# Kernel tuning notes

Measured on AMD Instinct MI355X. Metric: run time of the kernel, lower is better.

## Reference

```python
import jax, jax.numpy as jnp
import numpy as np

B, N, D, H, L = 16, 1024, 256, 128, 2  # batch, nodes, feat dim, gcn_hidden, n_layers (D == 2*H)


def setup_inputs() -> dict:
    key = jax.random.key(0)
    ks = jax.random.split(key, 16)
    inp = {
        "gcn_input": jax.random.normal(ks[0], (B, N, D), jnp.float32),
        # scale adjacencies by 1/N so aggregated features stay O(1)
        "latent_adj": jax.random.uniform(ks[1], (B, N, N), jnp.float32) / N,
        "dep_adj": jax.random.uniform(ks[2], (B, N, N), jnp.float32) / N,
        # stacked per-layer parameters (leading dim L); layers share shapes since D == 2*H
        "refine_gate": jax.random.normal(ks[3], (L, D, 1), jnp.float32) * 0.02,
        "gate_W_in": jax.random.normal(ks[4], (L, D, 1), jnp.float32) * 0.02,
        "gate_b_in": jnp.zeros((L, 1), jnp.float32),
        "gate_W_out": jax.random.normal(ks[5], (L, D, 1), jnp.float32) * 0.02,
        "gate_b_out": jnp.zeros((L, 1), jnp.float32),
        "fc_in_W": jax.random.normal(ks[6], (L, H, D), jnp.float32) * 0.02,
        "fc_in_b": jnp.zeros((L, H), jnp.float32),
        "fc_out_W": jax.random.normal(ks[7], (L, H, D), jnp.float32) * 0.02,
        "fc_out_b": jnp.zeros((L, H), jnp.float32),
        "ln_g": jnp.ones((L, 2 * H), jnp.float32),
        "ln_b": jnp.zeros((L, 2 * H), jnp.float32),
    }
    return inp


def _gcn_layer(x, latent, dep, rg, Wgi, bgi, Wgo, bgo, Wi, bi, Wo, bo, g, b):
    # refine gate blends dependency and latent adjacency per source node
    gate = jax.nn.sigmoid(x @ rg)  # [B,N,1]
    A_in = gate * dep + (1.0 - gate) * latent  # [B,N,N]
    A_out = gate * jnp.swapaxes(dep, -1, -2) + (1.0 - gate) * jnp.swapaxes(latent, -1, -2)
    Ax_in = A_in @ x   # [B,N,D]
    Ax_out = A_out @ x
    # gcn gates (scalar bias added after the gated product, as in torch)
    Ax_in = Ax_in * jax.nn.sigmoid(Ax_in @ Wgi) + bgi
    Ax_out = Ax_out * jax.nn.sigmoid(Ax_out @ Wgo) + bgo
    # rec_fc(Ax) + rec_fc(x): weight applied to sum, bias counted twice (faithful)
    h_in = (Ax_in + x) @ Wi.T + 2.0 * bi   # [B,N,H]
    h_out = (Ax_out + x) @ Wo.T + 2.0 * bo
    h = jnp.concatenate([h_in, h_out], axis=-1)  # [B,N,2H]
    mu = jnp.mean(h, axis=-1, keepdims=True)
    var = jnp.var(h, axis=-1, keepdims=True)
    h = (h - mu) * jax.lax.rsqrt(var + 1e-5) * g + b
    return jax.nn.gelu(h, approximate=False)


def reference(gcn_input, latent_adj, dep_adj, refine_gate, gate_W_in, gate_b_in,
              gate_W_out, gate_b_out, fc_in_W, fc_in_b, fc_out_W, fc_out_b, ln_g, ln_b):
    x = gcn_input
    for l in range(refine_gate.shape[0]):  # small fixed layer count
        x = _gcn_layer(x, latent_adj, dep_adj, refine_gate[l],
                       gate_W_in[l], gate_b_in[l], gate_W_out[l], gate_b_out[l],
                       fc_in_W[l], fc_in_b[l], fc_out_W[l], fc_out_b[l],
                       ln_g[l], ln_b[l])
    return x
```

## Files before the change

### kernel.cpp

```cpp
#include <hip/hip_runtime.h>
#include <hip/hip_bf16.h>
#include <cstdint>

#define B_ 16
#define N_ 1024
#define D_ 256
#define H_ 128

typedef unsigned short u16;
typedef __attribute__((ext_vector_type(8))) short bf16x8;
typedef __attribute__((ext_vector_type(4))) float f32x4;

__device__ __forceinline__ u16 f2bf(float f) {
    union { float f; uint32_t u; } v; v.f = f;
    return (u16)((v.u + 0x7FFFu + ((v.u >> 16) & 1u)) >> 16);
}

typedef __attribute__((address_space(3))) void lds_void;
typedef const __attribute__((address_space(1))) void g_void;

__device__ __forceinline__ void gl_lds16(const void* g, void* l) {
    __builtin_amdgcn_global_load_lds((g_void*)g, (lds_void*)l, 16, 0, 0);
}

__global__ __launch_bounds__(256) void k_conv_adj(
    const float* __restrict__ dep, const float* __restrict__ lat,
    u16* __restrict__ depb, u16* __restrict__ latb,
    u16* __restrict__ depTb, u16* __restrict__ latTb)
{
    __shared__ float tile[32][33];
    const int bz = blockIdx.z;
    const int b = bz >> 1;
    const float* src = (bz & 1) ? lat : dep;
    u16* dstN = (bz & 1) ? latb : depb;
    u16* dstT = (bz & 1) ? latTb : depTb;
    const int r0 = blockIdx.y * 32, c0 = blockIdx.x * 32;
    const int t = threadIdx.x;
    const int r = t >> 3, cg = (t & 7) * 4;

    const float4 v = *(const float4*)(src + ((size_t)b * N_ + r0 + r) * N_ + c0 + cg);
    ushort4 nv;
    nv.x = f2bf(v.x); nv.y = f2bf(v.y); nv.z = f2bf(v.z); nv.w = f2bf(v.w);
    *(ushort4*)(dstN + ((size_t)b * N_ + r0 + r) * N_ + c0 + cg) = nv;

    tile[r][cg] = v.x; tile[r][cg + 1] = v.y; tile[r][cg + 2] = v.z; tile[r][cg + 3] = v.w;
    __syncthreads();

    const int orow = t >> 3, ii = (t & 7) * 4;
    ushort4 tv;
    tv.x = f2bf(tile[ii][orow]);     tv.y = f2bf(tile[ii + 1][orow]);
    tv.z = f2bf(tile[ii + 2][orow]); tv.w = f2bf(tile[ii + 3][orow]);
    *(ushort4*)(dstT + ((size_t)b * N_ + c0 + orow) * N_ + r0 + ii) = tv;
}

__global__ __launch_bounds__(256) void k_gate_xt(
    const float* __restrict__ x, const float* __restrict__ rg,
    float* __restrict__ gate, u16* __restrict__ xT,
    const float* __restrict__ wi, const float* __restrict__ wo,
    u16* __restrict__ wib, u16* __restrict__ wob)
{
    if (blockIdx.y >= B_) {
        const int i = ((blockIdx.y - B_) * 32 + blockIdx.x) * 256 + threadIdx.x;
        wib[i] = f2bf(wi[i]);
        wob[i] = f2bf(wo[i]);
        return;
    }

    __shared__ u16 lx[D_][36];
    __shared__ float srg[D_];
    const int b = blockIdx.y, n0 = blockIdx.x * 32;
    const int t = threadIdx.x;
    srg[t] = rg[t];
    __syncthreads();

    const int r = t >> 3, cg = t & 7;
    const float* xrow = x + ((size_t)b * N_ + n0 + r) * D_;
    float dot = 0.f;
    #pragma unroll
    for (int u = 0; u < 8; ++u) {
        const int c = cg * 32 + u * 4;
        const float4 v = *(const float4*)(xrow + c);
        lx[c][r] = f2bf(v.x); lx[c + 1][r] = f2bf(v.y);
        lx[c + 2][r] = f2bf(v.z); lx[c + 3][r] = f2bf(v.w);
        dot += v.x * srg[c] + v.y * srg[c + 1] + v.z * srg[c + 2] + v.w * srg[c + 3];
    }
    dot += __shfl_down(dot, 4, 8);
    dot += __shfl_down(dot, 2, 8);
    dot += __shfl_down(dot, 1, 8);
    if (cg == 0) gate[(size_t)b * N_ + n0 + r] = 1.f / (1.f + expf(-dot));
    __syncthreads();

    #pragma unroll
    for (int i = 0; i < 8; ++i) {
        const int unit = i * 256 + t;
        const int d = unit >> 3, nch = (unit & 7) * 4;
        ushort4 wv;
        wv.x = lx[d][nch];     wv.y = lx[d][nch + 1];
        wv.z = lx[d][nch + 2]; wv.w = lx[d][nch + 3];
        *(ushort4*)(xT + ((size_t)b * D_ + d) * N_ + n0 + nch) = wv;
    }
}

__global__ __launch_bounds__(256, 4) void k_gemm_ax(
    const u16* __restrict__ depb, const u16* __restrict__ latb,
    const u16* __restrict__ depTb, const u16* __restrict__ latTb,
    const u16* __restrict__ xT,
    const float* __restrict__ gate,
    const float* __restrict__ Wgi, const float* __restrict__ Wgo,
    const float* __restrict__ bgi, const float* __restrict__ bgo,
    const float* __restrict__ xcur,
    u16* __restrict__ axin, u16* __restrict__ axout)
{
    __shared__ __align__(16) char smem[40960];
    float* hbuf = (float*)smem;
    float* sh_g = (float*)(smem + 33536);
    float* sh_s = (float*)(smem + 33664);

    const int bid = blockIdx.x;
    const int logical = (bid & 7) * 128 + (bid >> 3);
    const int b = logical >> 6;
    const int rem = logical & 63;
    const int z = rem >> 5;
    const int m0 = (rem & 31) * 32;

    const u16* A1 = z ? depTb : depb;
    const u16* A2 = z ? latTb : latb;
    const float* Wg = z ? Wgo : Wgi;
    const float bg0 = z ? bgo[0] : bgi[0];
    u16* outp = z ? axout : axin;

    const int t = threadIdx.x;
    const int lane = t & 63;
    const int w = t >> 6;

    f32x4 acc1[2][4], acc2[2][4];
    const f32x4 fz = {0.f, 0.f, 0.f, 0.f};
    #pragma unroll
    for (int i = 0; i < 2; ++i)
        #pragma unroll
        for (int j = 0; j < 4; ++j) { acc1[i][j] = fz; acc2[i][j] = fz; }

    const u16* gsrc[5];
    int loff[5];
    #pragma unroll
    for (int ci = 0; ci < 5; ++ci) {
        const int c = w * 5 + ci;
        const int el = lane * 8;
        if (c < 4) {
            const int cc = c & 1;
            const int e = cc * 512 + el;
            const int m = e >> 5, k = e & 31;
            const u16* base = (c < 2) ? A1 : A2;
            gsrc[ci] = base + ((size_t)b * N_ + m0 + m) * N_ + k;
            loff[ci] = ((c < 2) ? 0 : 1024) + cc * 512;
        } else {
            const int cc = c - 4;
            const int e = cc * 512 + el;
            const int n = e >> 5, k = e & 31;
            gsrc[ci] = xT + ((size_t)b * D_ + n) * N_ + k;
            loff[ci] = 2048 + cc * 512;
        }
    }

    u16* const sb0 = (u16*)smem;
    u16* const sb1 = sb0 + 10240;

    #pragma unroll
    for (int ci = 0; ci < 5; ++ci) gl_lds16(gsrc[ci], sb0 + loff[ci]);
    #pragma unroll
    for (int ci = 0; ci < 5; ++ci) gsrc[ci] += 32;

    const int mrow = lane & 15;
    const int kg = (lane >> 4) * 8;

    for (int ks = 0; ks < N_ / 32; ++ks) {
        __syncthreads();
        const u16* sc = (ks & 1) ? sb1 : sb0;
        u16* sn = (ks & 1) ? sb0 : sb1;
        if (ks < N_ / 32 - 1) {
            #pragma unroll
            for (int ci = 0; ci < 5; ++ci) gl_lds16(gsrc[ci], sn + loff[ci]);
            #pragma unroll
            for (int ci = 0; ci < 5; ++ci) gsrc[ci] += 32;
        }
        const u16* sA1 = sc;
        const u16* sA2 = sc + 1024;
        const u16* sB  = sc + 2048;
        bf16x8 a1[2], a2[2], fb[4];
        #pragma unroll
        for (int mt = 0; mt < 2; ++mt) {
            a1[mt] = *(const bf16x8*)(sA1 + (mt * 16 + mrow) * 32 + kg);
            a2[mt] = *(const bf16x8*)(sA2 + (mt * 16 + mrow) * 32 + kg);
        }
        #pragma unroll
        for (int nt = 0; nt < 4; ++nt)
            fb[nt] = *(const bf16x8*)(sB + (w * 64 + nt * 16 + mrow) * 32 + kg);
        #pragma unroll
        for (int mt = 0; mt < 2; ++mt)
            #pragma unroll
            for (int nt = 0; nt < 4; ++nt) {
                acc1[mt][nt] = __builtin_amdgcn_mfma_f32_16x16x32_bf16(a1[mt], fb[nt], acc1[mt][nt], 0, 0, 0);
                acc2[mt][nt] = __builtin_amdgcn_mfma_f32_16x16x32_bf16(a2[mt], fb[nt], acc2[mt][nt], 0, 0, 0);
            }
    }
    __syncthreads();

    if (t < 32) sh_g[t] = gate[(size_t)b * N_ + m0 + t];
    __syncthreads();

    const int hi = lane >> 4;
    #pragma unroll
    for (int mt = 0; mt < 2; ++mt)
        #pragma unroll
        for (int nt = 0; nt < 4; ++nt) {
            const int col = w * 64 + nt * 16 + mrow;
            #pragma unroll
            for (int rr = 0; rr < 4; ++rr) {
                const int row = mt * 16 + hi * 4 + rr;
                const float g = sh_g[row];
                hbuf[row * 260 + col] = g * acc1[mt][nt][rr] + (1.f - g) * acc2[mt][nt][rr];
            }
        }
    __syncthreads();

    {
        const int rr = t >> 3;
        const int c0 = (t & 7) * 32;
        float dot = 0.f;
        #pragma unroll 8
        for (int u = 0; u < 32; ++u) dot += hbuf[rr * 260 + c0 + u] * Wg[c0 + u];
        dot += __shfl_down(dot, 4, 8);
        dot += __shfl_down(dot, 2, 8);
        dot += __shfl_down(dot, 1, 8);
        if ((t & 7) == 0) sh_s[rr] = 1.f / (1.f + expf(-dot));
    }
    __syncthreads();

    #pragma unroll
    for (int i = 0; i < 16; ++i) {
        const int row = (t >> 7) + i * 2;
        const int c = (t & 127) * 2;
        const float s = sh_s[row];
        const size_t gidx = ((size_t)b * N_ + m0 + row) * D_ + c;
        const float2 xv = *(const float2*)(xcur + gidx);
        const float v0 = hbuf[row * 260 + c] * s + bg0 + xv.x;
        const float v1 = hbuf[row * 260 + c + 1] * s + bg0 + xv.y;
        *(ushort2*)(outp + gidx) = make_ushort2(f2bf(v0), f2bf(v1));
    }
}

__global__ __launch_bounds__(256, 4) void k_fc_ln(
    const u16* __restrict__ axin, const u16* __restrict__ axout,
    const u16* __restrict__ Wib, const u16* __restrict__ Wob,
    const float* __restrict__ bi, const float* __restrict__ bo,
    const float* __restrict__ lg, const float* __restrict__ lb,
    float* __restrict__ outp)
{
    __shared__ __align__(16) char smem[40960];
    float* hbuf = (float*)smem;
    float* sh_mu = (float*)(smem + 33536);
    float* sh_rs = (float*)(smem + 33664);

    const int b = blockIdx.y, m0 = blockIdx.x * 32;
    const int t = threadIdx.x, lane = t & 63, w = t >> 6;
    const int half = w >> 1, wn = w & 1;

    f32x4 acc[2][4];
    const f32x4 fz = {0.f, 0.f, 0.f, 0.f};
    #pragma unroll
    for (int i = 0; i < 2; ++i)
        #pragma unroll
        for (int j = 0; j < 4; ++j) acc[i][j] = fz;

    const u16* gsrc[5];
    int loff[5];
    #pragma unroll
    for (int ci = 0; ci < 5; ++ci) {
        const int c = w * 5 + ci;
        const int el = lane * 8;
        if (c < 4) {
            const int cc = c & 1;
            const int e = cc * 512 + el;
            const int m = e >> 5, k = e & 31;
            const u16* base = (c < 2) ? axin : axout;
            gsrc[ci] = base + ((size_t)b * N_ + m0 + m) * D_ + k;
            loff[ci] = ((c < 2) ? 0 : 1024) + cc * 512;
        } else {
            const int cc = (c - 4) & 7;
            const int e = cc * 512 + el;
            const int n = e >> 5, k = e & 31;
            const u16* base = (c < 12) ? Wib : Wob;
            gsrc[ci] = base + (size_t)n * D_ + k;
            loff[ci] = ((c < 12) ? 2048 : 6144) + cc * 512;
        }
    }

    u16* const sb0 = (u16*)smem;
    u16* const sb1 = sb0 + 10240;

    #pragma unroll
    for (int ci = 0; ci < 5; ++ci) gl_lds16(gsrc[ci], sb0 + loff[ci]);
    #pragma unroll
    for (int ci = 0; ci < 5; ++ci) gsrc[ci] += 32;

    const int mrow = lane & 15;
    const int kg = (lane >> 4) * 8;

    for (int ks = 0; ks < D_ / 32; ++ks) {
        __syncthreads();
        const u16* sc = (ks & 1) ? sb1 : sb0;
        u16* sn = (ks & 1) ? sb0 : sb1;
        if (ks < D_ / 32 - 1) {
            #pragma unroll
            for (int ci = 0; ci < 5; ++ci) gl_lds16(gsrc[ci], sn + loff[ci]);
            #pragma unroll
            for (int ci = 0; ci < 5; ++ci) gsrc[ci] += 32;
        }
        const u16* sA = sc + (half ? 1024 : 0);
        const u16* sW = sc + 2048 + (half ? 4096 : 0);
        bf16x8 a[2], fb[4];
        #pragma unroll
        for (int mt = 0; mt < 2; ++mt)
            a[mt] = *(const bf16x8*)(sA + (mt * 16 + mrow) * 32 + kg);
        #pragma unroll
        for (int nt = 0; nt < 4; ++nt)
            fb[nt] = *(const bf16x8*)(sW + (wn * 64 + nt * 16 + mrow) * 32 + kg);
        #pragma unroll
        for (int mt = 0; mt < 2; ++mt)
            #pragma unroll
            for (int nt = 0; nt < 4; ++nt)
                acc[mt][nt] = __builtin_amdgcn_mfma_f32_16x16x32_bf16(a[mt], fb[nt], acc[mt][nt], 0, 0, 0);
    }
    __syncthreads();

    const int hi = lane >> 4;
    #pragma unroll
    for (int mt = 0; mt < 2; ++mt)
        #pragma unroll
        for (int nt = 0; nt < 4; ++nt) {
            const int colh = wn * 64 + nt * 16 + mrow;
            const int col = half * 128 + colh;
            const float bias = 2.f * (half ? bo[colh] : bi[colh]);
            #pragma unroll
            for (int rr = 0; rr < 4; ++rr) {
                const int row = mt * 16 + hi * 4 + rr;
                hbuf[row * 260 + col] = acc[mt][nt][rr] + bias;
            }
        }
    __syncthreads();

    {
        const int rr = t >> 3;
        const int c0 = (t & 7) * 32;
        float s = 0.f, ss = 0.f;
        #pragma unroll 8
        for (int u = 0; u < 32; ++u) {
            const float v = hbuf[rr * 260 + c0 + u];
            s += v; ss += v * v;
        }
        s += __shfl_down(s, 4, 8);  ss += __shfl_down(ss, 4, 8);
        s += __shfl_down(s, 2, 8);  ss += __shfl_down(ss, 2, 8);
        s += __shfl_down(s, 1, 8);  ss += __shfl_down(ss, 1, 8);
        if ((t & 7) == 0) {
            const float mu = s * (1.f / 256.f);
            const float var = ss * (1.f / 256.f) - mu * mu;
            sh_mu[rr] = mu;
            sh_rs[rr] = rsqrtf(var + 1e-5f);
        }
    }
    __syncthreads();

    #pragma unroll
    for (int i = 0; i < 16; ++i) {
        const int row = (t >> 7) + i * 2;
        const int c = (t & 127) * 2;
        const float mu = sh_mu[row], rs = sh_rs[row];
        const float2 gg = *(const float2*)(lg + c);
        const float2 bb = *(const float2*)(lb + c);
        const float v0 = (hbuf[row * 260 + c] - mu) * rs * gg.x + bb.x;
        const float v1 = (hbuf[row * 260 + c + 1] - mu) * rs * gg.y + bb.y;
        const float y0 = 0.5f * v0 * (1.f + erff(v0 * 0.70710678118654752f));
        const float y1 = 0.5f * v1 * (1.f + erff(v1 * 0.70710678118654752f));
        const size_t gidx = ((size_t)b * N_ + m0 + row) * D_ + c;
        *(float2*)(outp + gidx) = make_float2(y0, y1);
    }
}

extern "C" void kernel_launch(void* const* d_in, const int* in_sizes, int n_in,
                              void* d_out, int out_size, void* d_ws, size_t ws_size,
                              hipStream_t stream)
{
    (void)in_sizes; (void)n_in; (void)out_size; (void)ws_size;

    const float* x0  = (const float*)d_in[0];
    const float* lat = (const float*)d_in[1];
    const float* dep = (const float*)d_in[2];
    const float* rg  = (const float*)d_in[3];
    const float* Wgi = (const float*)d_in[4];
    const float* bgi = (const float*)d_in[5];
    const float* Wgo = (const float*)d_in[6];
    const float* bgo = (const float*)d_in[7];
    const float* fiW = (const float*)d_in[8];
    const float* fib = (const float*)d_in[9];
    const float* foW = (const float*)d_in[10];
    const float* fob = (const float*)d_in[11];
    const float* lng = (const float*)d_in[12];
    const float* lnb = (const float*)d_in[13];

    char* ws = (char*)d_ws;
    size_t off = 0;
    auto alloc = [&](size_t bytes) {
        char* p = ws + off;
        off += (bytes + 255) & ~(size_t)255;
        return p;
    };
    u16* depb  = (u16*)alloc(2ull * B_ * N_ * N_);
    u16* latb  = (u16*)alloc(2ull * B_ * N_ * N_);
    u16* depTb = (u16*)alloc(2ull * B_ * N_ * N_);
    u16* latTb = (u16*)alloc(2ull * B_ * N_ * N_);
    u16* xT    = (u16*)alloc(2ull * B_ * D_ * N_);
    u16* axin  = (u16*)alloc(2ull * B_ * N_ * D_);
    u16* axout = (u16*)alloc(2ull * B_ * N_ * D_);
    float* gate = (float*)alloc(4ull * B_ * N_);
    float* xbuf = (float*)alloc(4ull * B_ * N_ * D_);
    u16* Wib = (u16*)alloc(2ull * H_ * D_);
    u16* Wob = (u16*)alloc(2ull * H_ * D_);

    k_conv_adj<<<dim3(32, 32, 32), 256, 0, stream>>>(dep, lat, depb, latb, depTb, latTb);

    const float* xcur = x0;
    for (int l = 0; l < 2; ++l) {
        k_gate_xt<<<dim3(32, B_ + 4), 256, 0, stream>>>(
            xcur, rg + l * D_, gate, xT,
            fiW + (size_t)l * H_ * D_, foW + (size_t)l * H_ * D_, Wib, Wob);
        k_gemm_ax<<<dim3(1024), 256, 0, stream>>>(
            depb, latb, depTb, latTb, xT, gate,
            Wgi + l * D_, Wgo + l * D_, bgi + l, bgo + l,
            xcur, axin, axout);
        const bool last = (l == 1);
        k_fc_ln<<<dim3(32, B_), 256, 0, stream>>>(
            axin, axout, Wib, Wob,
            fib + l * H_, fob + l * H_,
            lng + l * 2 * H_, lnb + l * 2 * H_,
            last ? (float*)d_out : xbuf);
        xcur = xbuf;
    }
}
```

Measured before the change: 357.0 us.

## Triple-buffer GEMM tiles with swizzled LDS and widen adjacency conversion tiles

Both MFMA GEMM kernels move from double to triple buffering of LDS tiles. They wait on vmcnt instead of a full syncthreads, so two tile loads stay in flight behind the compute. The LDS layout gets an XOR swizzle on the k-chunk to cut bank conflicts on the bf16x8 fragment reads. The adjacency conversion and transpose kernel now uses 64x64 tiles, bf16 in LDS and 16-byte stores. The cost is more LDS per block and occupancy lowered to 2 blocks, which could hurt latency hiding.

```diff
diff --git a/kernel.cpp b/kernel.cpp
--- a/kernel.cpp
+++ b/kernel.cpp
@@ -22,35 +22,62 @@
 __device__ __forceinline__ void gl_lds16(const void* g, void* l) {
     __builtin_amdgcn_global_load_lds((g_void*)g, (lds_void*)l, 16, 0, 0);
 }
+
+__device__ __forceinline__ void vm_wait5() { asm volatile("s_waitcnt vmcnt(5)" ::: "memory"); }
+__device__ __forceinline__ void vm_wait0() { asm volatile("s_waitcnt vmcnt(0)" ::: "memory"); }
 
 __global__ __launch_bounds__(256) void k_conv_adj(
     const float* __restrict__ dep, const float* __restrict__ lat,
     u16* __restrict__ depb, u16* __restrict__ latb,
     u16* __restrict__ depTb, u16* __restrict__ latTb)
 {
-    __shared__ float tile[32][33];
+    __shared__ u16 tile[64][64];
     const int bz = blockIdx.z;
     const int b = bz >> 1;
     const float* src = (bz & 1) ? lat : dep;
     u16* dstN = (bz & 1) ? latb : depb;
     u16* dstT = (bz & 1) ? latTb : depTb;
-    const int r0 = blockIdx.y * 32, c0 = blockIdx.x * 32;
+    const int r0 = blockIdx.y * 64, c0 = blockIdx.x * 64;
     const int t = threadIdx.x;
-    const int r = t >> 3, cg = (t & 7) * 4;
-
-    const float4 v = *(const float4*)(src + ((size_t)b * N_ + r0 + r) * N_ + c0 + cg);
-    ushort4 nv;
-    nv.x = f2bf(v.x); nv.y = f2bf(v.y); nv.z = f2bf(v.z); nv.w = f2bf(v.w);
-    *(ushort4*)(dstN + ((size_t)b * N_ + r0 + r) * N_ + c0 + cg) = nv;
-
-    tile[r][cg] = v.x; tile[r][cg + 1] = v.y; tile[r][cg + 2] = v.z; tile[r][cg + 3] = v.w;
-    __syncthreads();
-
-    const int orow = t >> 3, ii = (t & 7) * 4;
-    ushort4 tv;
-    tv.x = f2bf(tile[ii][orow]);     tv.y = f2bf(tile[ii + 1][orow]);
-    tv.z = f2bf(tile[ii + 2][orow]); tv.w = f2bf(tile[ii + 3][orow]);
-    *(ushort4*)(dstT + ((size_t)b * N_ + c0 + orow) * N_ + r0 + ii) = tv;
+    const int r = t >> 2, cg = (t & 3) * 16;
+
+    const float* srow = src + ((size_t)b * N_ + r0 + r) * N_ + c0 + cg;
+    bf16x8 lo, hi;
+    {
+        const float4 v0 = *(const float4*)(srow);
+        const float4 v1 = *(const float4*)(srow + 4);
+        const float4 v2 = *(const float4*)(srow + 8);
+        const float4 v3 = *(const float4*)(srow + 12);
+        lo[0] = (short)f2bf(v0.x); lo[1] = (short)f2bf(v0.y); lo[2] = (short)f2bf(v0.z); lo[3] = (short)f2bf(v0.w);
+        lo[4] = (short)f2bf(v1.x); lo[5] = (short)f2bf(v1.y); lo[6] = (short)f2bf(v1.z); lo[7] = (short)f2bf(v1.w);
+        hi[0] = (short)f2bf(v2.x); hi[1] = (short)f2bf(v2.y); hi[2] = (short)f2bf(v2.z); hi[3] = (short)f2bf(v2.w);
+        hi[4] = (short)f2bf(v3.x); hi[5] = (short)f2bf(v3.y); hi[6] = (short)f2bf(v3.z); hi[7] = (short)f2bf(v3.w);
+    }
+    u16* nrow = dstN + ((size_t)b * N_ + r0 + r) * N_ + c0 + cg;
+    *(bf16x8*)nrow = lo;
+    *(bf16x8*)(nrow + 8) = hi;
+
+    const int g0 = (t & 3) * 2;
+    const int s = r & 7;
+    *(bf16x8*)(&tile[r][((g0    ) ^ s) * 8]) = lo;
+    *(bf16x8*)(&tile[r][((g0 + 1) ^ s) * 8]) = hi;
+    __syncthreads();
+
+    const int sc = t >> 2, rg2 = (t & 3) * 16;
+    bf16x8 o0, o1;
+    #pragma unroll
+    for (int i = 0; i < 8; ++i) {
+        const int R = rg2 + i;
+        o0[i] = (short)tile[R][(((sc >> 3) ^ (R & 7)) * 8) + (sc & 7)];
+    }
+    #pragma unroll
+    for (int i = 0; i < 8; ++i) {
+        const int R = rg2 + 8 + i;
+        o1[i] = (short)tile[R][(((sc >> 3) ^ (R & 7)) * 8) + (sc & 7)];
+    }
+    u16* dT = dstT + ((size_t)b * N_ + c0 + sc) * N_ + r0 + rg2;
+    *(bf16x8*)dT = o0;
+    *(bf16x8*)(dT + 8) = o1;
 }
 
 __global__ __launch_bounds__(256) void k_gate_xt(
@@ -101,7 +128,7 @@
     }
 }
 
-__global__ __launch_bounds__(256, 4) void k_gemm_ax(
+__global__ __launch_bounds__(256, 2) void k_gemm_ax(
     const u16* __restrict__ depb, const u16* __restrict__ latb,
     const u16* __restrict__ depTb, const u16* __restrict__ latTb,
     const u16* __restrict__ xT,
@@ -111,10 +138,10 @@
     const float* __restrict__ xcur,
     u16* __restrict__ axin, u16* __restrict__ axout)
 {
-    __shared__ __align__(16) char smem[40960];
+    __shared__ __align__(16) char smem[61696];
     float* hbuf = (float*)smem;
-    float* sh_g = (float*)(smem + 33536);
-    float* sh_s = (float*)(smem + 33664);
+    float* sh_g = (float*)(smem + 61440);
+    float* sh_s = (float*)(smem + 61568);
 
     const int bid = blockIdx.x;
     const int logical = (bid & 7) * 128 + (bid >> 3);
@@ -142,59 +169,60 @@
 
     const u16* gsrc[5];
     int loff[5];
+    const int rl = lane >> 2;
+    const int kk = (((lane & 3) ^ ((lane >> 3) & 3)) << 3);
     #pragma unroll
     for (int ci = 0; ci < 5; ++ci) {
         const int c = w * 5 + ci;
-        const int el = lane * 8;
         if (c < 4) {
             const int cc = c & 1;
-            const int e = cc * 512 + el;
-            const int m = e >> 5, k = e & 31;
+            const int m = cc * 16 + rl;
             const u16* base = (c < 2) ? A1 : A2;
-            gsrc[ci] = base + ((size_t)b * N_ + m0 + m) * N_ + k;
+            gsrc[ci] = base + ((size_t)b * N_ + m0 + m) * N_ + kk;
             loff[ci] = ((c < 2) ? 0 : 1024) + cc * 512;
         } else {
             const int cc = c - 4;
-            const int e = cc * 512 + el;
-            const int n = e >> 5, k = e & 31;
-            gsrc[ci] = xT + ((size_t)b * D_ + n) * N_ + k;
+            const int n = cc * 16 + rl;
+            gsrc[ci] = xT + ((size_t)b * D_ + n) * N_ + kk;
             loff[ci] = 2048 + cc * 512;
         }
     }
 
-    u16* const sb0 = (u16*)smem;
-    u16* const sb1 = sb0 + 10240;
-
-    #pragma unroll
-    for (int ci = 0; ci < 5; ++ci) gl_lds16(gsrc[ci], sb0 + loff[ci]);
-    #pragma unroll
-    for (int ci = 0; ci < 5; ++ci) gsrc[ci] += 32;
+    u16* const sb = (u16*)smem;
+
+    #pragma unroll
+    for (int ci = 0; ci < 5; ++ci) gl_lds16(gsrc[ci], sb + loff[ci]);
+    #pragma unroll
+    for (int ci = 0; ci < 5; ++ci) { gl_lds16(gsrc[ci] + 32, sb + 10240 + loff[ci]); gsrc[ci] += 64; }
 
     const int mrow = lane & 15;
-    const int kg = (lane >> 4) * 8;
+    const int kg = (((lane >> 4) ^ ((mrow >> 1) & 3)) << 3);
 
     for (int ks = 0; ks < N_ / 32; ++ks) {
-        __syncthreads();
-        const u16* sc = (ks & 1) ? sb1 : sb0;
-        u16* sn = (ks & 1) ? sb0 : sb1;
-        if (ks < N_ / 32 - 1) {
-            #pragma unroll
-            for (int ci = 0; ci < 5; ++ci) gl_lds16(gsrc[ci], sn + loff[ci]);
-            #pragma unroll
-            for (int ci = 0; ci < 5; ++ci) gsrc[ci] += 32;
-        }
-        const u16* sA1 = sc;
-        const u16* sA2 = sc + 1024;
-        const u16* sB  = sc + 2048;
+        if (ks == 31) vm_wait0(); else vm_wait5();
+        __builtin_amdgcn_s_barrier();
+        __builtin_amdgcn_sched_barrier(0);
+        if (ks <= 29) {
+            u16* nb = sb + ((ks + 2) % 3) * 10240;
+            #pragma unroll
+            for (int ci = 0; ci < 5; ++ci) { gl_lds16(gsrc[ci], nb + loff[ci]); gsrc[ci] += 32; }
+        }
+        const u16* cur = sb + (ks % 3) * 10240;
+        const u16* sA1 = cur;
+        const u16* sA2 = cur + 1024;
+        const u16* sB  = cur + 2048;
         bf16x8 a1[2], a2[2], fb[4];
         #pragma unroll
         for (int mt = 0; mt < 2; ++mt) {
-            a1[mt] = *(const bf16x8*)(sA1 + (mt * 16 + mrow) * 32 + kg);
-            a2[mt] = *(const bf16x8*)(sA2 + (mt * 16 + mrow) * 32 + kg);
-        }
-        #pragma unroll
-        for (int nt = 0; nt < 4; ++nt)
-            fb[nt] = *(const bf16x8*)(sB + (w * 64 + nt * 16 + mrow) * 32 + kg);
+            const int row = mt * 16 + mrow;
+            a1[mt] = *(const bf16x8*)(sA1 + row * 32 + kg);
+            a2[mt] = *(const bf16x8*)(sA2 + row * 32 + kg);
+        }
+        #pragma unroll
+        for (int nt = 0; nt < 4; ++nt) {
+            const int row = w * 64 + nt * 16 + mrow;
+            fb[nt] = *(const bf16x8*)(sB + row * 32 + kg);
+        }
         #pragma unroll
         for (int mt = 0; mt < 2; ++mt)
             #pragma unroll
@@ -249,17 +277,17 @@
     }
 }
 
-__global__ __launch_bounds__(256, 4) void k_fc_ln(
+__global__ __launch_bounds__(256, 2) void k_fc_ln(
     const u16* __restrict__ axin, const u16* __restrict__ axout,
     const u16* __restrict__ Wib, const u16* __restrict__ Wob,
     const float* __restrict__ bi, const float* __restrict__ bo,
     const float* __restrict__ lg, const float* __restrict__ lb,
     float* __restrict__ outp)
 {
-    __shared__ __align__(16) char smem[40960];
+    __shared__ __align__(16) char smem[61696];
     float* hbuf = (float*)smem;
-    float* sh_mu = (float*)(smem + 33536);
-    float* sh_rs = (float*)(smem + 33664);
+    float* sh_mu = (float*)(smem + 61440);
+    float* sh_rs = (float*)(smem + 61568);
 
     const int b = blockIdx.y, m0 = blockIdx.x * 32;
     const int t = threadIdx.x, lane = t & 63, w = t >> 6;
@@ -274,50 +302,48 @@
 
     const u16* gsrc[5];
     int loff[5];
+    const int rl = lane >> 2;
+    const int kk = (((lane & 3) ^ ((lane >> 3) & 3)) << 3);
     #pragma unroll
     for (int ci = 0; ci < 5; ++ci) {
         const int c = w * 5 + ci;
-        const int el = lane * 8;
         if (c < 4) {
             const int cc = c & 1;
-            const int e = cc * 512 + el;
-            const int m = e >> 5, k = e & 31;
+            const int m = cc * 16 + rl;
             const u16* base = (c < 2) ? axin : axout;
-            gsrc[ci] = base + ((size_t)b * N_ + m0 + m) * D_ + k;
+            gsrc[ci] = base + ((size_t)b * N_ + m0 + m) * D_ + kk;
             loff[ci] = ((c < 2) ? 0 : 1024) + cc * 512;
         } else {
             const int cc = (c - 4) & 7;
-            const int e = cc * 512 + el;
-            const int n = e >> 5, k = e & 31;
+            const int n = cc * 16 + rl;
             const u16* base = (c < 12) ? Wib : Wob;
-            gsrc[ci] = base + (size_t)n * D_ + k;
+            gsrc[ci] = base + (size_t)n * D_ + kk;
             loff[ci] = ((c < 12) ? 2048 : 6144) + cc * 512;
         }
     }
 
-    u16* const sb0 = (u16*)smem;
-    u16* const sb1 = sb0 + 10240;
-
-    #pragma unroll
-    for (int ci = 0; ci < 5; ++ci) gl_lds16(gsrc[ci], sb0 + loff[ci]);
-    #pragma unroll
-    for (int ci = 0; ci < 5; ++ci) gsrc[ci] += 32;
+    u16* const sb = (u16*)smem;
+
+    #pragma unroll
+    for (int ci = 0; ci < 5; ++ci) gl_lds16(gsrc[ci], sb + loff[ci]);
+    #pragma unroll
+    for (int ci = 0; ci < 5; ++ci) { gl_lds16(gsrc[ci] + 32, sb + 10240 + loff[ci]); gsrc[ci] += 64; }
 
     const int mrow = lane & 15;
-    const int kg = (lane >> 4) * 8;
+    const int kg = (((lane >> 4) ^ ((mrow >> 1) & 3)) << 3);
 
     for (int ks = 0; ks < D_ / 32; ++ks) {
-        __syncthreads();
-        const u16* sc = (ks & 1) ? sb1 : sb0;
-        u16* sn = (ks & 1) ? sb0 : sb1;
-        if (ks < D_ / 32 - 1) {
-            #pragma unroll
-            for (int ci = 0; ci < 5; ++ci) gl_lds16(gsrc[ci], sn + loff[ci]);
-            #pragma unroll
-            for (int ci = 0; ci < 5; ++ci) gsrc[ci] += 32;
-        }
-        const u16* sA = sc + (half ? 1024 : 0);
-        const u16* sW = sc + 2048 + (half ? 4096 : 0);
+        if (ks == 7) vm_wait0(); else vm_wait5();
+        __builtin_amdgcn_s_barrier();
+        __builtin_amdgcn_sched_barrier(0);
+        if (ks <= 5) {
+            u16* nb = sb + ((ks + 2) % 3) * 10240;
+            #pragma unroll
+            for (int ci = 0; ci < 5; ++ci) { gl_lds16(gsrc[ci], nb + loff[ci]); gsrc[ci] += 32; }
+        }
+        const u16* cur = sb + (ks % 3) * 10240;
+        const u16* sA = cur + (half ? 1024 : 0);
+        const u16* sW = cur + 2048 + (half ? 4096 : 0);
         bf16x8 a[2], fb[4];
         #pragma unroll
         for (int mt = 0; mt < 2; ++mt)
@@ -426,7 +452,7 @@
     u16* Wib = (u16*)alloc(2ull * H_ * D_);
     u16* Wob = (u16*)alloc(2ull * H_ * D_);
 
-    k_conv_adj<<<dim3(32, 32, 32), 256, 0, stream>>>(dep, lat, depb, latb, depTb, latTb);
+    k_conv_adj<<<dim3(16, 16, 32), 256, 0, stream>>>(dep, lat, depb, latb, depTb, latTb);
 
     const float* xcur = x0;
     for (int l = 0; l < 2; ++l) {
```

After: 352.6 us. About the same (-1.2%).
